# Optimization experiments

Measured on AMD Instinct MI355X. Metric: run time of the kernel, lower is better.

The kernel has to match this reference:

```python
import jax, jax.numpy as jnp
import numpy as np
import math

B, S, D = 1, 2048, 2048
NQ, NKV = 32, 8
HD = D // NQ            # 64
NREP = NQ // NKV        # 4
EPS = 1e-6


def _rope_tables(seq_len, head_dim, theta=10000.0):
    half = head_dim // 2
    inv_freq = 1.0 / (theta ** (np.arange(0, half, dtype=np.float32) / half))
    t = np.arange(seq_len, dtype=np.float32)
    freqs = np.outer(t, inv_freq)  # [S, half]
    return jnp.asarray(np.cos(freqs)), jnp.asarray(np.sin(freqs))


def _rmsnorm(x, g, eps=EPS):
    denom = jnp.sqrt(jnp.mean(x * x, axis=-1, keepdims=True) + eps)
    return x / denom * g


def _rope(x, cos, sin):
    # x: [B, S, H, HD]; cos/sin: [S, HD//2]
    half = x.shape[-1] // 2
    x1, x2 = x[..., :half], x[..., half:]
    c = cos[None, :, None, :]
    s = sin[None, :, None, :]
    return jnp.concatenate([x1 * c - x2 * s, x1 * s + x2 * c], axis=-1)


def setup_inputs() -> dict:
    key = jax.random.key(0)
    ks = jax.random.split(key, 6)
    scale = 1.0 / math.sqrt(D)
    x = jax.random.normal(ks[0], (B, S, D), dtype=jnp.float32)
    Wq = jax.random.normal(ks[1], (D, NQ * HD), dtype=jnp.float32) * scale
    Wk = jax.random.normal(ks[2], (D, NKV * HD), dtype=jnp.float32) * scale
    Wv = jax.random.normal(ks[3], (D, NKV * HD), dtype=jnp.float32) * scale
    Wo = jax.random.normal(ks[4], (NQ * HD, D), dtype=jnp.float32) * scale
    g_q = jnp.ones((HD,), dtype=jnp.float32)
    g_k = jnp.ones((HD,), dtype=jnp.float32)
    cos, sin = _rope_tables(S, HD)
    return {"x": x, "cos": cos, "sin": sin, "g_q": g_q, "g_k": g_k,
            "Wq": Wq, "Wk": Wk, "Wv": Wv, "Wo": Wo}


def reference(x, cos, sin, g_q, g_k, Wq, Wk, Wv, Wo):
    bs, seq, _ = x.shape
    Q = (x @ Wq).reshape(bs, seq, NQ, HD)
    K = (x @ Wk).reshape(bs, seq, NKV, HD)
    V = (x @ Wv).reshape(bs, seq, NKV, HD)
    Q = _rope(_rmsnorm(Q, g_q), cos, sin)
    K = _rope(_rmsnorm(K, g_k), cos, sin)
    # GQA: repeat_interleave KV heads to match Q heads
    K = jnp.repeat(K, NREP, axis=2)  # [B,S,NQ,HD]
    V = jnp.repeat(V, NREP, axis=2)
    # scores: [B, H, S, S]
    scores = jnp.einsum('bshd,bthd->bhst', Q, K) / math.sqrt(HD)
    mask = jnp.triu(jnp.ones((seq, seq), dtype=bool), k=1)
    scores = jnp.where(mask, -jnp.inf, scores)
    attn = jax.nn.softmax(scores, axis=-1)
    out = jnp.einsum('bhst,bthd->bshd', attn, V).reshape(bs, seq, NQ * HD)
    return out @ Wo
```

## Files before the change

### kernel.cpp

```cpp
#include <hip/hip_runtime.h>
#include <hip/hip_bf16.h>
#include <math.h>

#define S 2048
#define D 2048
#define NQ 32
#define NKV 8
#define HD 64
#define HALF 32
#define NREP 4
#define QKV_N 3072
#define KCOL 2048
#define VCOL 2560

typedef unsigned short ushort_t;
typedef __attribute__((ext_vector_type(8))) short bf16x8;
typedef __attribute__((ext_vector_type(4))) float f32x4;
typedef float f4 __attribute__((ext_vector_type(4)));

__device__ __forceinline__ ushort_t f2bf(float f) {
    __hip_bfloat16 h = __float2bfloat16(f);
    return *reinterpret_cast<ushort_t*>(&h);
}
__device__ __forceinline__ float bf2f(ushort_t u) {
    __hip_bfloat16 h = *reinterpret_cast<__hip_bfloat16*>(&u);
    return __bfloat162float(h);
}

__device__ __forceinline__ void load_lds16(const ushort_t* g, ushort_t* l) {
    __builtin_amdgcn_global_load_lds(
        (const __attribute__((address_space(1))) unsigned int*)g,
        (__attribute__((address_space(3))) unsigned int*)l,
        16, 0, 0);
}

__global__ __launch_bounds__(256) void convert_bf16(const float* __restrict__ src,
                                                    ushort_t* __restrict__ dst, int n) {
    int i = (blockIdx.x * 256 + threadIdx.x) * 4;
    if (i + 3 < n) {
        f4 v = *(const f4*)&src[i];
        dst[i + 0] = f2bf(v[0]);
        dst[i + 1] = f2bf(v[1]);
        dst[i + 2] = f2bf(v[2]);
        dst[i + 3] = f2bf(v[3]);
    }
}

__global__ __launch_bounds__(256) void transpose_w(const float* __restrict__ src,
                                                   ushort_t* __restrict__ dst,
                                                   int Kdim, int N, int pitch, int row_off) {
    __shared__ float tile[32][33];
    const int n0 = blockIdx.x * 32, k0 = blockIdx.y * 32;
    const int tx = threadIdx.x & 31, ty = threadIdx.x >> 5;
    #pragma unroll
    for (int i = 0; i < 32; i += 8)
        tile[ty + i][tx] = src[(size_t)(k0 + ty + i) * N + (n0 + tx)];
    __syncthreads();
    #pragma unroll
    for (int i = 0; i < 32; i += 8)
        dst[(size_t)(row_off + n0 + ty + i) * pitch + (k0 + tx)] = f2bf(tile[tx][ty + i]);
}

__global__ __launch_bounds__(256) void transpose_v(const ushort_t* __restrict__ src,
                                                   ushort_t* __restrict__ dst) {
    __shared__ ushort_t tile[32][33];
    const int s0 = blockIdx.x * 32, d0 = blockIdx.y * 32;
    const int tx = threadIdx.x & 31, ty = threadIdx.x >> 5;
    #pragma unroll
    for (int i = 0; i < 32; i += 8)
        tile[ty + i][tx] = src[(size_t)(s0 + ty + i) * QKV_N + VCOL + d0 + tx];
    __syncthreads();
    #pragma unroll
    for (int i = 0; i < 32; i += 8)
        dst[(size_t)(d0 + ty + i) * S + s0 + tx] = tile[tx][ty + i];
}

template <typename OutT>
__global__ __launch_bounds__(256) void gemm_bt(const ushort_t* __restrict__ A,
                                               const ushort_t* __restrict__ BT,
                                               OutT* __restrict__ C,
                                               int M, int N, int Kdim) {
    __shared__ ushort_t As[128][32];
    __shared__ ushort_t Bs[128][32];
    const int tid = threadIdx.x;
    const int w = tid >> 6, lane = tid & 63;
    const int r16 = lane & 15, quad = lane >> 4;
    const int wm = (w >> 1) * 64, wn = (w & 1) * 64;
    const int bm = blockIdx.y * 128, bn = blockIdx.x * 128;
    const int sr = lane >> 2;
    const int sc8 = (lane & 3) * 8;

    f32x4 acc[4][4];
    #pragma unroll
    for (int r = 0; r < 4; ++r)
        #pragma unroll
        for (int c = 0; c < 4; ++c) acc[r][c] = (f32x4){0.f, 0.f, 0.f, 0.f};

    for (int k0 = 0; k0 < Kdim; k0 += 32) {
        __syncthreads();
        #pragma unroll
        for (int i = 0; i < 2; ++i) {
            int rowt = w * 32 + i * 16;
            load_lds16(A  + (size_t)(bm + rowt + sr) * Kdim + k0 + sc8, &As[rowt][0]);
            load_lds16(BT + (size_t)(bn + rowt + sr) * Kdim + k0 + sc8, &Bs[rowt][0]);
        }
        __syncthreads();

        bf16x8 af[4], bfr[4];
        #pragma unroll
        for (int r = 0; r < 4; ++r) af[r]  = *(const bf16x8*)&As[wm + 16 * r + r16][quad * 8];
        #pragma unroll
        for (int c = 0; c < 4; ++c) bfr[c] = *(const bf16x8*)&Bs[wn + 16 * c + r16][quad * 8];
        #pragma unroll
        for (int r = 0; r < 4; ++r)
            #pragma unroll
            for (int c = 0; c < 4; ++c)
                acc[r][c] = __builtin_amdgcn_mfma_f32_16x16x32_bf16(af[r], bfr[c], acc[r][c], 0, 0, 0);
    }

    #pragma unroll
    for (int r = 0; r < 4; ++r)
        #pragma unroll
        for (int c = 0; c < 4; ++c)
            #pragma unroll
            for (int reg = 0; reg < 4; ++reg) {
                int row = bm + wm + 16 * r + quad * 4 + reg;
                int col = bn + wn + 16 * c + r16;
                float v = acc[r][c][reg];
                if constexpr (sizeof(OutT) == 2) C[(size_t)row * N + col] = (OutT)f2bf(v);
                else                             C[(size_t)row * N + col] = (OutT)v;
            }
}

__global__ __launch_bounds__(256) void rmsnorm_rope_b(ushort_t* __restrict__ QKV,
                                                      const float* __restrict__ gq,
                                                      const float* __restrict__ gk,
                                                      const float* __restrict__ cosT,
                                                      const float* __restrict__ sinT) {
    const int s = blockIdx.x;
    const int w = threadIdx.x >> 6;
    const int hh = blockIdx.y * 4 + w;
    const int d = threadIdx.x & 63;
    const float* g;
    int col;
    if (hh < NQ) { g = gq; col = hh * HD; }
    else         { g = gk; col = KCOL + (hh - NQ) * HD; }

    ushort_t* xp = QKV + (size_t)s * QKV_N + col;
    float v = bf2f(xp[d]);
    float ss = v * v;
    #pragma unroll
    for (int off = 32; off > 0; off >>= 1) ss += __shfl_down(ss, off);
    ss = __shfl(ss, 0);
    float inv = rsqrtf(ss * (1.0f / HD) + 1e-6f);
    float xn = v * inv * g[d];

    float other = __shfl(xn, d ^ 32);
    float c = cosT[(size_t)s * HALF + (d & 31)];
    float sn = sinT[(size_t)s * HALF + (d & 31)];
    float outv = (d < HALF) ? (xn * c - other * sn) : (other * sn + xn * c);
    xp[d] = f2bf(outv);
}

__global__ __launch_bounds__(256) void flash_attn_mfma(const ushort_t* __restrict__ QKV,
                                                       const ushort_t* __restrict__ VTg,
                                                       ushort_t* __restrict__ O) {
    __shared__ ushort_t Ks[2][64][64];
    __shared__ ushort_t Vt[2][64][64];
    __shared__ ushort_t Ps[4][16][72];

    const int qt = gridDim.x - 1 - blockIdx.x;
    const int q0 = qt * 64;
    const int h  = blockIdx.y;
    const int kvh = h >> 2;
    const int tid = threadIdx.x;
    const int w = tid >> 6, lane = tid & 63;
    const int r16 = lane & 15, quad = lane >> 4;
    const int kcol = KCOL + kvh * HD;
    const int vtrow0 = kvh * HD;
    const int rsub = lane >> 3;
    const int jlog = (lane & 7) ^ rsub;
    const int rx = r16 & 7;

    const ushort_t* qrow = QKV + (size_t)(q0 + 16 * w + r16) * QKV_N + h * HD;
    bf16x8 qf0, qf1;
    {
        bf16x8 r0 = *(const bf16x8*)(qrow + quad * 8);
        bf16x8 r1 = *(const bf16x8*)(qrow + quad * 8 + 32);
        #pragma unroll
        for (int j = 0; j < 8; ++j) {
            qf0[j] = (short)f2bf(bf2f((ushort_t)r0[j]) * 0.18033688f);
            qf1[j] = (short)f2bf(bf2f((ushort_t)r1[j]) * 0.18033688f);
        }
    }

    bf16x8 onesf;
    {
        ushort_t ov = (r16 == 0) ? (ushort_t)0x3F80 : (ushort_t)0;
        #pragma unroll
        for (int j = 0; j < 8; ++j) onesf[j] = (short)ov;
    }

    f32x4 accO[4];
    f32x4 accL = (f32x4){0.f, 0.f, 0.f, 0.f};
    #pragma unroll
    for (int c = 0; c < 4; ++c) accO[c] = (f32x4){0.f, 0.f, 0.f, 0.f};

    auto stage = [&](int b, int t0) {
        #pragma unroll
        for (int i = 0; i < 2; ++i) {
            int base = w * 16 + i * 8;
            int row = base + rsub;
            load_lds16(QKV + (size_t)(t0 + row) * QKV_N + kcol + jlog * 8, &Ks[b][base][0]);
            load_lds16(VTg + (size_t)(vtrow0 + row) * S + t0 + jlog * 8, &Vt[b][base][0]);
        }
    };

    const int ntiles = qt + 1;
    stage(0, 0);

    for (int t = 0; t < ntiles; ++t) {
        __syncthreads();
        if (t + 1 < ntiles) stage((t + 1) & 1, (t + 1) * 64);

        const ushort_t (*K_)[64] = Ks[t & 1];
        const ushort_t (*V_)[64] = Vt[t & 1];
        const bool diag = (t == qt);

        f32x4 sc[4];
        #pragma unroll
        for (int c = 0; c < 4; ++c) {
            bf16x8 kf0 = *(const bf16x8*)&K_[16 * c + r16][(quad ^ rx) * 8];
            bf16x8 kf1 = *(const bf16x8*)&K_[16 * c + r16][((quad + 4) ^ rx) * 8];
            f32x4 z = (f32x4){0.f, 0.f, 0.f, 0.f};
            z = __builtin_amdgcn_mfma_f32_16x16x32_bf16(qf0, kf0, z, 0, 0, 0);
            z = __builtin_amdgcn_mfma_f32_16x16x32_bf16(qf1, kf1, z, 0, 0, 0);
            sc[c] = z;
        }

        #pragma unroll
        for (int c = 0; c < 4; ++c)
            #pragma unroll
            for (int reg = 0; reg < 4; ++reg) {
                float v = sc[c][reg];
                if (diag && (16 * c + r16 > 16 * w + quad * 4 + reg)) v = -INFINITY;
                float p = exp2f(v);
                Ps[w][quad * 4 + reg][16 * c + r16] = f2bf(p);
            }

        bf16x8 pf0 = *(const bf16x8*)&Ps[w][r16][quad * 8];
        bf16x8 pf1 = *(const bf16x8*)&Ps[w][r16][quad * 8 + 32];

        accL = __builtin_amdgcn_mfma_f32_16x16x32_bf16(pf0, onesf, accL, 0, 0, 0);
        accL = __builtin_amdgcn_mfma_f32_16x16x32_bf16(pf1, onesf, accL, 0, 0, 0);

        #pragma unroll
        for (int c = 0; c < 4; ++c) {
            bf16x8 vf0 = *(const bf16x8*)&V_[16 * c + r16][(quad ^ rx) * 8];
            bf16x8 vf1 = *(const bf16x8*)&V_[16 * c + r16][((quad + 4) ^ rx) * 8];
            accO[c] = __builtin_amdgcn_mfma_f32_16x16x32_bf16(pf0, vf0, accO[c], 0, 0, 0);
            accO[c] = __builtin_amdgcn_mfma_f32_16x16x32_bf16(pf1, vf1, accO[c], 0, 0, 0);
        }
    }

    #pragma unroll
    for (int reg = 0; reg < 4; ++reg) {
        float l = __shfl(accL[reg], lane & 48);
        float invl = 1.0f / l;
        int row = q0 + 16 * w + quad * 4 + reg;
        ushort_t* op = O + (size_t)row * D + h * HD;
        #pragma unroll
        for (int c = 0; c < 4; ++c)
            op[16 * c + r16] = f2bf(accO[c][reg] * invl);
    }
}

extern "C" void kernel_launch(void* const* d_in, const int* in_sizes, int n_in,
                              void* d_out, int out_size, void* d_ws, size_t ws_size,
                              hipStream_t stream) {
    const float* x    = (const float*)d_in[0];
    const float* cosT = (const float*)d_in[1];
    const float* sinT = (const float*)d_in[2];
    const float* g_q  = (const float*)d_in[3];
    const float* g_k  = (const float*)d_in[4];
    const float* Wq   = (const float*)d_in[5];
    const float* Wk   = (const float*)d_in[6];
    const float* Wv   = (const float*)d_in[7];
    const float* Wo   = (const float*)d_in[8];
    float* out = (float*)d_out;

    char* base = (char*)d_ws;
    ushort_t* Xb    = (ushort_t*)base;
    ushort_t* WqkvT = (ushort_t*)(base + 8388608);
    ushort_t* QKVb  = (ushort_t*)(base + 20971520);
    ushort_t* WoT   = (ushort_t*)(base + 8388608);
    ushort_t* VTg   = (ushort_t*)(base + 16777216);
    ushort_t* Ob    = Xb;

    convert_bf16<<<(S * D) / 1024, 256, 0, stream>>>(x, Xb, S * D);
    transpose_w<<<dim3(2048 / 32, 2048 / 32), 256, 0, stream>>>(Wq, WqkvT, 2048, 2048, 2048, 0);
    transpose_w<<<dim3(512 / 32, 2048 / 32), 256, 0, stream>>>(Wk, WqkvT, 2048, 512, 2048, 2048);
    transpose_w<<<dim3(512 / 32, 2048 / 32), 256, 0, stream>>>(Wv, WqkvT, 2048, 512, 2048, 2560);
    gemm_bt<ushort_t><<<dim3(QKV_N / 128, S / 128), 256, 0, stream>>>(Xb, WqkvT, QKVb, S, QKV_N, D);
    rmsnorm_rope_b<<<dim3(S, 10), 256, 0, stream>>>(QKVb, g_q, g_k, cosT, sinT);
    transpose_v<<<dim3(S / 32, 512 / 32), 256, 0, stream>>>(QKVb, VTg);
    transpose_w<<<dim3(2048 / 32, 2048 / 32), 256, 0, stream>>>(Wo, WoT, 2048, 2048, 2048, 0);
    flash_attn_mfma<<<dim3(S / 64, NQ), 256, 0, stream>>>(QKVb, VTg, Ob);
    gemm_bt<float><<<dim3(D / 128, S / 128), 256, 0, stream>>>(Ob, WoT, out, S, D, D);
}
```

Measured before the change: 310.5 us.

## Split long causal attention rows across blocks and halve GEMM M-tile

Query tiles 16-31 are split into two KV ranges, each handled by a separate block. Partial unnormalized outputs and row sums go into an fp32 buffer via atomicAdd, and a new normalize kernel finishes those tiles. This balances the causal workload across 48 blocks per head instead of 32 uneven ones. Both GEMMs also move to a 64x128 tile to get more blocks, at the cost of lower per-block reuse. It adds zeroing kernels, atomic traffic and extra launches, and the ordering of the Wo transpose is adjusted so the accumulation buffer can reuse the weight workspace.

```diff
diff --git a/kernel.cpp b/kernel.cpp
--- a/kernel.cpp
+++ b/kernel.cpp
@@ -46,6 +46,11 @@
     }
 }
 
+__global__ __launch_bounds__(256) void zero_f32(f4* __restrict__ p, int n4) {
+    int i = blockIdx.x * 256 + threadIdx.x;
+    if (i < n4) p[i] = (f4){0.f, 0.f, 0.f, 0.f};
+}
+
 __global__ __launch_bounds__(256) void transpose_w(const float* __restrict__ src,
                                                    ushort_t* __restrict__ dst,
                                                    int Kdim, int N, int pitch, int row_off) {
@@ -76,50 +81,49 @@
 }
 
 template <typename OutT>
-__global__ __launch_bounds__(256) void gemm_bt(const ushort_t* __restrict__ A,
-                                               const ushort_t* __restrict__ BT,
-                                               OutT* __restrict__ C,
-                                               int M, int N, int Kdim) {
-    __shared__ ushort_t As[128][32];
+__global__ __launch_bounds__(256) void gemm_bt64(const ushort_t* __restrict__ A,
+                                                 const ushort_t* __restrict__ BT,
+                                                 OutT* __restrict__ C,
+                                                 int M, int N, int Kdim) {
+    __shared__ ushort_t As[64][32];
     __shared__ ushort_t Bs[128][32];
     const int tid = threadIdx.x;
     const int w = tid >> 6, lane = tid & 63;
     const int r16 = lane & 15, quad = lane >> 4;
-    const int wm = (w >> 1) * 64, wn = (w & 1) * 64;
-    const int bm = blockIdx.y * 128, bn = blockIdx.x * 128;
+    const int wm = (w >> 1) * 32, wn = (w & 1) * 64;
+    const int bm = blockIdx.y * 64, bn = blockIdx.x * 128;
     const int sr = lane >> 2;
     const int sc8 = (lane & 3) * 8;
 
-    f32x4 acc[4][4];
-    #pragma unroll
-    for (int r = 0; r < 4; ++r)
+    f32x4 acc[2][4];
+    #pragma unroll
+    for (int r = 0; r < 2; ++r)
         #pragma unroll
         for (int c = 0; c < 4; ++c) acc[r][c] = (f32x4){0.f, 0.f, 0.f, 0.f};
 
     for (int k0 = 0; k0 < Kdim; k0 += 32) {
         __syncthreads();
-        #pragma unroll
-        for (int i = 0; i < 2; ++i) {
-            int rowt = w * 32 + i * 16;
-            load_lds16(A  + (size_t)(bm + rowt + sr) * Kdim + k0 + sc8, &As[rowt][0]);
-            load_lds16(BT + (size_t)(bn + rowt + sr) * Kdim + k0 + sc8, &Bs[rowt][0]);
-        }
+        load_lds16(A + (size_t)(bm + w * 16 + sr) * Kdim + k0 + sc8, &As[w * 16][0]);
+        #pragma unroll
+        for (int i = 0; i < 2; ++i)
+            load_lds16(BT + (size_t)(bn + w * 32 + i * 16 + sr) * Kdim + k0 + sc8,
+                       &Bs[w * 32 + i * 16][0]);
         __syncthreads();
 
-        bf16x8 af[4], bfr[4];
-        #pragma unroll
-        for (int r = 0; r < 4; ++r) af[r]  = *(const bf16x8*)&As[wm + 16 * r + r16][quad * 8];
+        bf16x8 af[2], bfr[4];
+        #pragma unroll
+        for (int r = 0; r < 2; ++r) af[r]  = *(const bf16x8*)&As[wm + 16 * r + r16][quad * 8];
         #pragma unroll
         for (int c = 0; c < 4; ++c) bfr[c] = *(const bf16x8*)&Bs[wn + 16 * c + r16][quad * 8];
         #pragma unroll
-        for (int r = 0; r < 4; ++r)
+        for (int r = 0; r < 2; ++r)
             #pragma unroll
             for (int c = 0; c < 4; ++c)
                 acc[r][c] = __builtin_amdgcn_mfma_f32_16x16x32_bf16(af[r], bfr[c], acc[r][c], 0, 0, 0);
     }
 
     #pragma unroll
-    for (int r = 0; r < 4; ++r)
+    for (int r = 0; r < 2; ++r)
         #pragma unroll
         for (int c = 0; c < 4; ++c)
             #pragma unroll
@@ -164,12 +168,19 @@
 
 __global__ __launch_bounds__(256) void flash_attn_mfma(const ushort_t* __restrict__ QKV,
                                                        const ushort_t* __restrict__ VTg,
-                                                       ushort_t* __restrict__ O) {
+                                                       ushort_t* __restrict__ O,
+                                                       float* __restrict__ AccBuf,
+                                                       float* __restrict__ AccL) {
     __shared__ ushort_t Ks[2][64][64];
     __shared__ ushort_t Vt[2][64][64];
     __shared__ ushort_t Ps[4][16][72];
 
-    const int qt = gridDim.x - 1 - blockIdx.x;
+    const int bx = blockIdx.x;
+    int qt, tb, te;
+    bool atom;
+    if (bx < 16) { qt = 16 + bx; tb = 0; te = 16; atom = true; }
+    else         { qt = 47 - bx; atom = (qt >= 16); tb = atom ? 16 : 0; te = qt + 1; }
+
     const int q0 = qt * 64;
     const int h  = blockIdx.y;
     const int kvh = h >> 2;
@@ -216,12 +227,11 @@
         }
     };
 
-    const int ntiles = qt + 1;
-    stage(0, 0);
-
-    for (int t = 0; t < ntiles; ++t) {
+    stage(tb & 1, tb * 64);
+
+    for (int t = tb; t < te; ++t) {
         __syncthreads();
-        if (t + 1 < ntiles) stage((t + 1) & 1, (t + 1) * 64);
+        if (t + 1 < te) stage((t + 1) & 1, (t + 1) * 64);
 
         const ushort_t (*K_)[64] = Ks[t & 1];
         const ushort_t (*V_)[64] = Vt[t & 1];
@@ -263,15 +273,46 @@
         }
     }
 
-    #pragma unroll
-    for (int reg = 0; reg < 4; ++reg) {
-        float l = __shfl(accL[reg], lane & 48);
-        float invl = 1.0f / l;
-        int row = q0 + 16 * w + quad * 4 + reg;
-        ushort_t* op = O + (size_t)row * D + h * HD;
-        #pragma unroll
-        for (int c = 0; c < 4; ++c)
-            op[16 * c + r16] = f2bf(accO[c][reg] * invl);
+    if (!atom) {
+        #pragma unroll
+        for (int reg = 0; reg < 4; ++reg) {
+            float l = __shfl(accL[reg], lane & 48);
+            float invl = 1.0f / l;
+            int row = q0 + 16 * w + quad * 4 + reg;
+            ushort_t* op = O + (size_t)row * D + h * HD;
+            #pragma unroll
+            for (int c = 0; c < 4; ++c)
+                op[16 * c + r16] = f2bf(accO[c][reg] * invl);
+        }
+    } else {
+        const int pair = (qt - 16) * 32 + h;
+        float* ab = AccBuf + (size_t)pair * 4096;
+        #pragma unroll
+        for (int reg = 0; reg < 4; ++reg) {
+            int row = 16 * w + quad * 4 + reg;
+            #pragma unroll
+            for (int c = 0; c < 4; ++c)
+                atomicAdd(&ab[row * 64 + 16 * c + r16], accO[c][reg]);
+        }
+        if (r16 == 0) {
+            #pragma unroll
+            for (int reg = 0; reg < 4; ++reg)
+                atomicAdd(&AccL[pair * 64 + 16 * w + quad * 4 + reg], accL[reg]);
+        }
+    }
+}
+
+__global__ __launch_bounds__(256) void normalize_o(const float* __restrict__ AccBuf,
+                                                   const float* __restrict__ AccL,
+                                                   ushort_t* __restrict__ O) {
+    const int pair = blockIdx.x;
+    const int qt = 16 + (pair >> 5);
+    const int h  = pair & 31;
+    const float* ab = AccBuf + (size_t)pair * 4096;
+    const float* lp = AccL + pair * 64;
+    for (int i = threadIdx.x; i < 4096; i += 256) {
+        int row = i >> 6, d = i & 63;
+        O[(size_t)(qt * 64 + row) * D + h * HD + d] = f2bf(ab[i] / lp[row]);
     }
 }
 
@@ -290,21 +331,26 @@
     float* out = (float*)d_out;
 
     char* base = (char*)d_ws;
-    ushort_t* Xb    = (ushort_t*)base;
-    ushort_t* WqkvT = (ushort_t*)(base + 8388608);
-    ushort_t* QKVb  = (ushort_t*)(base + 20971520);
-    ushort_t* WoT   = (ushort_t*)(base + 8388608);
-    ushort_t* VTg   = (ushort_t*)(base + 16777216);
-    ushort_t* Ob    = Xb;
+    ushort_t* Xb     = (ushort_t*)base;
+    ushort_t* WqkvT  = (ushort_t*)(base + 8388608);
+    ushort_t* QKVb   = (ushort_t*)(base + 20971520);
+    float*    AccBuf = (float*)(base + 8388608);
+    ushort_t* WoT    = (ushort_t*)(base + 8388608);
+    ushort_t* VTg    = (ushort_t*)(base + 16777216);
+    float*    AccL   = (float*)(base + 18874368);
+    ushort_t* Ob     = Xb;
 
     convert_bf16<<<(S * D) / 1024, 256, 0, stream>>>(x, Xb, S * D);
     transpose_w<<<dim3(2048 / 32, 2048 / 32), 256, 0, stream>>>(Wq, WqkvT, 2048, 2048, 2048, 0);
     transpose_w<<<dim3(512 / 32, 2048 / 32), 256, 0, stream>>>(Wk, WqkvT, 2048, 512, 2048, 2048);
     transpose_w<<<dim3(512 / 32, 2048 / 32), 256, 0, stream>>>(Wv, WqkvT, 2048, 512, 2048, 2560);
-    gemm_bt<ushort_t><<<dim3(QKV_N / 128, S / 128), 256, 0, stream>>>(Xb, WqkvT, QKVb, S, QKV_N, D);
+    gemm_bt64<ushort_t><<<dim3(QKV_N / 128, S / 64), 256, 0, stream>>>(Xb, WqkvT, QKVb, S, QKV_N, D);
     rmsnorm_rope_b<<<dim3(S, 10), 256, 0, stream>>>(QKVb, g_q, g_k, cosT, sinT);
     transpose_v<<<dim3(S / 32, 512 / 32), 256, 0, stream>>>(QKVb, VTg);
+    zero_f32<<<(2097152 / 4 + 255) / 256, 256, 0, stream>>>((f4*)AccBuf, 2097152 / 4);
+    zero_f32<<<(32768 / 4 + 255) / 256, 256, 0, stream>>>((f4*)AccL, 32768 / 4);
+    flash_attn_mfma<<<dim3(48, NQ), 256, 0, stream>>>(QKVb, VTg, Ob, AccBuf, AccL);
+    normalize_o<<<512, 256, 0, stream>>>(AccBuf, AccL, Ob);
     transpose_w<<<dim3(2048 / 32, 2048 / 32), 256, 0, stream>>>(Wo, WoT, 2048, 2048, 2048, 0);
-    flash_attn_mfma<<<dim3(S / 64, NQ), 256, 0, stream>>>(QKVb, VTg, Ob);
-    gemm_bt<float><<<dim3(D / 128, S / 128), 256, 0, stream>>>(Ob, WoT, out, S, D, D);
-}
+    gemm_bt64<float><<<dim3(D / 128, S / 64), 256, 0, stream>>>(Ob, WoT, out, S, D, D);
+}
```

New measurement: 282.1 us. 9.2% less time.
